# Kernel optimization log

Measured on AMD Instinct MI355X. Metric: run time of the kernel, lower is better.

## Reference

```python
import jax, jax.numpy as jnp
import numpy as np

NUM_NODES = 50000
NUM_EDGES = 800000
INPUT_DIM = 128
HIDDEN_DIM = 128
PE_DIM = 64


def setup_inputs() -> dict:
    key = jax.random.key(0)
    ks = jax.random.split(key, 12)
    x = jax.random.normal(ks[0], (NUM_NODES, INPUT_DIM), dtype=jnp.float32)
    edge_index = jax.random.randint(ks[1], (2, NUM_EDGES), 0, NUM_NODES, dtype=jnp.int64)
    edge_pe = jax.random.normal(ks[2], (NUM_EDGES, PE_DIM), dtype=jnp.float32)
    # message_net: Linear(input+pe -> hidden), ReLU, Linear(hidden -> hidden)
    s1 = 1.0 / np.sqrt(INPUT_DIM + PE_DIM)
    W1 = jax.random.uniform(ks[3], (INPUT_DIM + PE_DIM, HIDDEN_DIM), minval=-s1, maxval=s1)
    b1 = jax.random.uniform(ks[4], (HIDDEN_DIM,), minval=-s1, maxval=s1)
    s2 = 1.0 / np.sqrt(HIDDEN_DIM)
    W2 = jax.random.uniform(ks[5], (HIDDEN_DIM, HIDDEN_DIM), minval=-s2, maxval=s2)
    b2 = jax.random.uniform(ks[6], (HIDDEN_DIM,), minval=-s2, maxval=s2)
    # update_net: Linear(input+hidden -> hidden), ReLU, Linear(hidden -> input)
    s3 = 1.0 / np.sqrt(INPUT_DIM + HIDDEN_DIM)
    U1 = jax.random.uniform(ks[7], (INPUT_DIM + HIDDEN_DIM, HIDDEN_DIM), minval=-s3, maxval=s3)
    c1 = jax.random.uniform(ks[8], (HIDDEN_DIM,), minval=-s3, maxval=s3)
    U2 = jax.random.uniform(ks[9], (HIDDEN_DIM, INPUT_DIM), minval=-s2, maxval=s2)
    c2 = jax.random.uniform(ks[10], (INPUT_DIM,), minval=-s2, maxval=s2)
    return {"x": x, "edge_pe": edge_pe, "W1": W1, "b1": b1, "W2": W2, "b2": b2,
            "U1": U1, "c1": c1, "U2": U2, "c2": c2, "edge_index": edge_index}


def reference(x, edge_pe, W1, b1, W2, b2, U1, c1, U2, c2, edge_index):
    src, dst = edge_index[0], edge_index[1]
    # gather source node features per edge: [E, input_dim]
    msg_in = jnp.concatenate([x[src], edge_pe], axis=-1)  # [E, input+pe]
    h = jax.nn.relu(msg_in @ W1 + b1)
    messages = h @ W2 + b2  # [E, hidden]
    # scatter-add messages to destination nodes
    aggregated = jax.ops.segment_sum(messages, dst, num_segments=x.shape[0])  # [N, hidden]
    upd_in = jnp.concatenate([x, aggregated], axis=-1)  # [N, input+hidden]
    u = jax.nn.relu(upd_in @ U1 + c1)
    return u @ U2 + c2  # [N, input_dim]
```

## Files before the change

kernel.cpp:

```cpp
#include <hip/hip_runtime.h>

#define NN 50000
#define NE 800000

typedef __attribute__((ext_vector_type(8))) short bf16x8;
typedef __attribute__((ext_vector_type(4))) float f32x4;

#define SWS(s, kt) ((s) ^ (((s) >> 3) & 6) ^ ((kt) & 3))

__device__ __forceinline__ unsigned cvtpk(float lo, float hi) {
    unsigned r;
    asm("v_cvt_pk_bf16_f32 %0, %1, %2" : "=v"(r) : "v"(lo), "v"(hi));
    return r;
}
__device__ __forceinline__ uint2 pack4(float a, float b, float c, float d) {
    return make_uint2(cvtpk(a, b), cvtpk(c, d));
}

__device__ __forceinline__ void prep_weights_body(int tid,
        const float* __restrict__ W1, const float* __restrict__ W2,
        const float* __restrict__ U1, const float* __restrict__ U2,
        unsigned short* __restrict__ ws) {
    const float* src; unsigned short* dst; int K;
    if (tid < 6144)        { src = W1; dst = ws;         K = 192; }
    else if (tid < 10240)  { tid -= 6144;  src = W2; dst = ws + 24576; K = 128; }
    else if (tid < 18432)  { tid -= 10240; src = U1; dst = ws + 40960; K = 256; }
    else if (tid < 22528)  { tid -= 18432; src = U2; dst = ws + 73728; K = 128; }
    else return;
    const int m = tid & 127, k = (tid >> 7) * 4;
    const int KT = K >> 5;
    uint2 p = pack4(src[(k + 0) * 128 + m], src[(k + 1) * 128 + m],
                    src[(k + 2) * 128 + m], src[(k + 3) * 128 + m]);
    const int mt = m >> 4, kt = k >> 5, lane = (m & 15) + (((k & 31) >> 3) << 4);
    const int off = (((mt * KT + kt) << 9) + (lane << 3) + ((k & 4) ? 4 : 0));
    *reinterpret_cast<uint2*>(dst + off) = p;
}

__global__ __launch_bounds__(256)
void prep_all(const float* __restrict__ W1, const float* __restrict__ W2,
              const float* __restrict__ U1, const float* __restrict__ U2,
              const float* __restrict__ x, const int* __restrict__ ei,
              unsigned short* __restrict__ ws, unsigned short* __restrict__ xb,
              int* __restrict__ counts) {
    const int b = blockIdx.x;
    if (b < 88) {
        prep_weights_body(b * 256 + threadIdx.x, W1, W2, U1, U2, ws);
    } else if (b < 3213) {
        const int i = ((b - 88) * 256 + threadIdx.x) * 8;
        if (i >= NN * 128) return;
        const float4 a = *reinterpret_cast<const float4*>(&x[i]);
        const float4 c = *reinterpret_cast<const float4*>(&x[i + 4]);
        *reinterpret_cast<uint4*>(&xb[i]) =
            make_uint4(cvtpk(a.x, a.y), cvtpk(a.z, a.w), cvtpk(c.x, c.y), cvtpk(c.z, c.w));
    } else {
        const int e = (b - 3213) * 256 + threadIdx.x;
        if (e < NE) atomicAdd(&counts[ei[NE + e]], 1);
    }
}

__global__ void prep_weights(const float* __restrict__ W1, const float* __restrict__ W2,
                             const float* __restrict__ U1, const float* __restrict__ U2,
                             unsigned short* __restrict__ ws) {
    prep_weights_body(blockIdx.x * blockDim.x + threadIdx.x, W1, W2, U1, U2, ws);
}

__global__ void hist_kernel(const int* __restrict__ ei, int* __restrict__ counts) {
    const int e = blockIdx.x * blockDim.x + threadIdx.x;
    if (e < NE) atomicAdd(&counts[ei[NE + e]], 1);
}

__global__ __launch_bounds__(256)
void scan1_kernel(const int* __restrict__ counts, int* __restrict__ offs,
                  int* __restrict__ bsums) {
    __shared__ int wsum[4];
    const int t = threadIdx.x, lane = t & 63, w = t >> 6;
    const int i = blockIdx.x * 256 + t;
    const int v = (i < NN) ? counts[i] : 0;
    int s = v;
#pragma unroll
    for (int d = 1; d < 64; d <<= 1) {
        int u = __shfl_up(s, d, 64);
        if (lane >= d) s += u;
    }
    if (lane == 63) wsum[w] = s;
    __syncthreads();
    if (t == 0) {
        int a = 0;
#pragma unroll
        for (int k = 0; k < 4; ++k) { int tmp = wsum[k]; wsum[k] = a; a += tmp; }
    }
    __syncthreads();
    const int excl = wsum[w] + s - v;
    if (i < NN) offs[i] = excl;
    if (t == 255) bsums[blockIdx.x] = wsum[3] + s;
}

__global__ __launch_bounds__(256)
void scan2_kernel(const int* __restrict__ bsums, int* __restrict__ boffs) {
    __shared__ int wsum[4];
    const int t = threadIdx.x, lane = t & 63, w = t >> 6;
    const int v = (t < 196) ? bsums[t] : 0;
    int s = v;
#pragma unroll
    for (int d = 1; d < 64; d <<= 1) {
        int u = __shfl_up(s, d, 64);
        if (lane >= d) s += u;
    }
    if (lane == 63) wsum[w] = s;
    __syncthreads();
    if (t == 0) {
        int a = 0;
#pragma unroll
        for (int k = 0; k < 4; ++k) { int tmp = wsum[k]; wsum[k] = a; a += tmp; }
    }
    __syncthreads();
    boffs[t] = wsum[w] + s - v;
}

__global__ __launch_bounds__(256)
void scan3_kernel(int* __restrict__ offs, const int* __restrict__ boffs,
                  int* __restrict__ cursor) {
    const int i = blockIdx.x * 256 + threadIdx.x;
    if (i < NN) {
        const int o = offs[i] + boffs[i >> 8];
        offs[i] = o;
        cursor[i] = o;
    }
}

__global__ void fill_kernel(const int* __restrict__ ei, int* __restrict__ cursor,
                            int* __restrict__ csrpos) {
    const int e = blockIdx.x * blockDim.x + threadIdx.x;
    if (e < NE) csrpos[e] = atomicAdd(&cursor[ei[NE + e]], 1);
}

template <int XBF>
__global__ __launch_bounds__(512)
void edge_kernel2(const float* __restrict__ x,
                  const unsigned short* __restrict__ xb,
                  const float* __restrict__ pe,
                  const float* __restrict__ b1,
                  const float* __restrict__ b2,
                  const int* __restrict__ ei,
                  const int* __restrict__ csrpos,
                  const unsigned short* __restrict__ wf,
                  unsigned short* __restrict__ msg)
{
    __shared__ __align__(16) unsigned char Asw[24576];
    __shared__ __align__(16) unsigned char Hsw[16384];

    const int t = threadIdx.x;
    const int l = t & 63;
    const int w = t >> 6;
    const int g = l >> 4;

    bf16x8 w1r[6], w2r[4];
    {
        const bf16x8* wp1 = reinterpret_cast<const bf16x8*>(wf);
        const bf16x8* wp2 = reinterpret_cast<const bf16x8*>(wf + 24576);
#pragma unroll
        for (int kt = 0; kt < 6; ++kt) w1r[kt] = wp1[(w * 6 + kt) * 64 + l];
#pragma unroll
        for (int kt = 0; kt < 4; ++kt) w2r[kt] = wp2[(w * 4 + kt) * 64 + l];
    }
    const float4 b1v = *reinterpret_cast<const float4*>(&b1[16 * w + 4 * g]);
    const float4 b2v = *reinterpret_cast<const float4*>(&b2[16 * w + 4 * g]);

    const int le = t >> 3;
    const int sub = t & 7;
    const int nt_s = le >> 4;
    const int lane_s = (le & 15) + ((sub & 3) << 4);

    uint4  rxb[2];
    float4 rxf[4];
    float4 rpf[2];

    const int tile0 = blockIdx.x * 5;

    {
        const int e0 = tile0 * 64;
        const int src = ei[e0 + le];
        if constexpr (XBF) {
#pragma unroll
            for (int j = 0; j < 2; ++j)
                rxb[j] = *reinterpret_cast<const uint4*>(&xb[(size_t)src * 128 + sub * 8 + 64 * j]);
        } else {
#pragma unroll
            for (int j = 0; j < 2; ++j) {
                rxf[2 * j]     = *reinterpret_cast<const float4*>(&x[(size_t)src * 128 + sub * 8 + 64 * j]);
                rxf[2 * j + 1] = *reinterpret_cast<const float4*>(&x[(size_t)src * 128 + sub * 8 + 64 * j + 4]);
            }
        }
        rpf[0] = *reinterpret_cast<const float4*>(&pe[(size_t)(e0 + le) * 64 + sub * 8]);
        rpf[1] = *reinterpret_cast<const float4*>(&pe[(size_t)(e0 + le) * 64 + sub * 8 + 4]);
    }

    for (int ti = 0; ti < 5; ++ti) {
        const int e0 = (tile0 + ti) * 64;
        int cp[4];
#pragma unroll
        for (int nt = 0; nt < 4; ++nt) cp[nt] = csrpos[e0 + nt * 16 + (l & 15)];

        __syncthreads();

        {
#pragma unroll
            for (int j = 0; j < 2; ++j) {
                const int kt = (sub >> 2) + 2 * j;
                uint4 v;
                if constexpr (XBF) v = rxb[j];
                else v = make_uint4(cvtpk(rxf[2 * j].x, rxf[2 * j].y), cvtpk(rxf[2 * j].z, rxf[2 * j].w),
                                    cvtpk(rxf[2 * j + 1].x, rxf[2 * j + 1].y), cvtpk(rxf[2 * j + 1].z, rxf[2 * j + 1].w));
                *reinterpret_cast<uint4*>(Asw + ((kt * 4 + nt_s) << 10) + (SWS(lane_s, kt) << 4)) = v;
            }
            const int ktp = 4 + (sub >> 2);
            *reinterpret_cast<uint4*>(Asw + ((ktp * 4 + nt_s) << 10) + (SWS(lane_s, ktp) << 4)) =
                make_uint4(cvtpk(rpf[0].x, rpf[0].y), cvtpk(rpf[0].z, rpf[0].w),
                           cvtpk(rpf[1].x, rpf[1].y), cvtpk(rpf[1].z, rpf[1].w));
        }

        if (ti < 4) {
            const int e0n = e0 + 64;
            const int srcn = ei[e0n + le];
            if constexpr (XBF) {
#pragma unroll
                for (int j = 0; j < 2; ++j)
                    rxb[j] = *reinterpret_cast<const uint4*>(&xb[(size_t)srcn * 128 + sub * 8 + 64 * j]);
            } else {
#pragma unroll
                for (int j = 0; j < 2; ++j) {
                    rxf[2 * j]     = *reinterpret_cast<const float4*>(&x[(size_t)srcn * 128 + sub * 8 + 64 * j]);
                    rxf[2 * j + 1] = *reinterpret_cast<const float4*>(&x[(size_t)srcn * 128 + sub * 8 + 64 * j + 4]);
                }
            }
            rpf[0] = *reinterpret_cast<const float4*>(&pe[(size_t)(e0n + le) * 64 + sub * 8]);
            rpf[1] = *reinterpret_cast<const float4*>(&pe[(size_t)(e0n + le) * 64 + sub * 8 + 4]);
        }

        __syncthreads();

        f32x4 acc[4];
#pragma unroll
        for (int nt = 0; nt < 4; ++nt) acc[nt] = (f32x4){0.f, 0.f, 0.f, 0.f};
#pragma unroll
        for (int kt = 0; kt < 6; ++kt) {
#pragma unroll
            for (int nt = 0; nt < 4; ++nt) {
                const bf16x8 af = *reinterpret_cast<const bf16x8*>(
                    Asw + ((kt * 4 + nt) << 10) + (SWS(l, kt) << 4));
                acc[nt] = __builtin_amdgcn_mfma_f32_16x16x32_bf16(w1r[kt], af, acc[nt], 0, 0, 0);
            }
        }

        {
            const int kt2 = (16 * w + 4 * g) >> 5;
            const int lane2 = (l & 15) + ((2 * (w & 1) + (g >> 1)) << 4);
            const int bo = (g & 1) << 3;
#pragma unroll
            for (int nt = 0; nt < 4; ++nt) {
                float v0 = fmaxf(acc[nt][0] + b1v.x, 0.f);
                float v1 = fmaxf(acc[nt][1] + b1v.y, 0.f);
                float v2 = fmaxf(acc[nt][2] + b1v.z, 0.f);
                float v3 = fmaxf(acc[nt][3] + b1v.w, 0.f);
                *reinterpret_cast<uint2*>(Hsw + ((kt2 * 4 + nt) << 10) + (SWS(lane2, kt2) << 4) + bo) =
                    make_uint2(cvtpk(v0, v1), cvtpk(v2, v3));
            }
        }

        __syncthreads();

#pragma unroll
        for (int nt = 0; nt < 4; ++nt) acc[nt] = (f32x4){0.f, 0.f, 0.f, 0.f};
#pragma unroll
        for (int kt = 0; kt < 4; ++kt) {
#pragma unroll
            for (int nt = 0; nt < 4; ++nt) {
                const bf16x8 hf = *reinterpret_cast<const bf16x8*>(
                    Hsw + ((kt * 4 + nt) << 10) + (SWS(l, kt) << 4));
                acc[nt] = __builtin_amdgcn_mfma_f32_16x16x32_bf16(w2r[kt], hf, acc[nt], 0, 0, 0);
            }
        }

        const int mbase = 16 * w + 4 * g;
#pragma unroll
        for (int nt = 0; nt < 4; ++nt) {
            *reinterpret_cast<uint2*>(&msg[(size_t)cp[nt] * 128 + mbase]) =
                make_uint2(cvtpk(acc[nt][0] + b2v.x, acc[nt][1] + b2v.y),
                           cvtpk(acc[nt][2] + b2v.z, acc[nt][3] + b2v.w));
        }
    }
}

template <int XBF>
__global__ __launch_bounds__(512)
void node_fused(const float* __restrict__ x,
                const unsigned short* __restrict__ xb,
                const float* __restrict__ c1,
                const float* __restrict__ c2,
                const unsigned short* __restrict__ wf,
                const int* __restrict__ offs,
                const int* __restrict__ counts,
                const unsigned short* __restrict__ msg,
                float* __restrict__ out)
{
    __shared__ __align__(16) unsigned char Asw[32768];
    __shared__ __align__(16) unsigned char Hsw[16384];

    const int t = threadIdx.x;
    const int l = t & 63;
    const int w = t >> 6;
    const int g = l >> 4;

    bf16x8 u1r[8], u2r[4];
    {
        const bf16x8* up1 = reinterpret_cast<const bf16x8*>(wf + 40960);
        const bf16x8* up2 = reinterpret_cast<const bf16x8*>(wf + 73728);
#pragma unroll
        for (int kt = 0; kt < 8; ++kt) u1r[kt] = up1[(w * 8 + kt) * 64 + l];
#pragma unroll
        for (int kt = 0; kt < 4; ++kt) u2r[kt] = up2[(w * 4 + kt) * 64 + l];
    }
    const float4 c1v = *reinterpret_cast<const float4*>(&c1[16 * w + 4 * g]);
    const float4 c2v = *reinterpret_cast<const float4*>(&c2[16 * w + 4 * g]);

    const int n0 = blockIdx.x * 64;
    const int le = t >> 3;
    const int q  = t & 7;
    const int nt_s = le >> 4;
    const int node = n0 + le;
    const bool valid = node < NN;

    float a16[16];
#pragma unroll
    for (int i = 0; i < 16; ++i) a16[i] = 0.f;
    int start = 0, cnt = 0;
    if (valid) { start = offs[node]; cnt = counts[node]; }
    for (int j = 0; j < cnt; ++j) {
        const uint4* mp = reinterpret_cast<const uint4*>(&msg[(size_t)(start + j) * 128 + q * 16]);
        const uint4 u0 = mp[0], u1 = mp[1];
        const unsigned arr[8] = {u0.x, u0.y, u0.z, u0.w, u1.x, u1.y, u1.z, u1.w};
#pragma unroll
        for (int r = 0; r < 8; ++r) {
            union { unsigned u; float f; } lo, hi;
            lo.u = arr[r] << 16;
            hi.u = arr[r] & 0xFFFF0000u;
            a16[2 * r]     += lo.f;
            a16[2 * r + 1] += hi.f;
        }
    }

#pragma unroll
    for (int i = 0; i < 2; ++i) {
        const int o = 2 * q + i;
        const int kt = o >> 2;
        const int slot = (le & 15) + ((o & 3) << 4);
        uint4 v = make_uint4(0u, 0u, 0u, 0u);
        if (valid) {
            if constexpr (XBF) {
                v = *reinterpret_cast<const uint4*>(&xb[(size_t)node * 128 + o * 8]);
            } else {
                const float4 f0 = *reinterpret_cast<const float4*>(&x[(size_t)node * 128 + o * 8]);
                const float4 f1 = *reinterpret_cast<const float4*>(&x[(size_t)node * 128 + o * 8 + 4]);
                v = make_uint4(cvtpk(f0.x, f0.y), cvtpk(f0.z, f0.w),
                               cvtpk(f1.x, f1.y), cvtpk(f1.z, f1.w));
            }
        }
        *reinterpret_cast<uint4*>(Asw + ((kt * 4 + nt_s) << 10) + (SWS(slot, kt) << 4)) = v;
    }

    {
        const int kt = 4 + (q >> 1);
#pragma unroll
        for (int i = 0; i < 2; ++i) {
            const int j4 = 2 * (q & 1) + i;
            const int slot = (le & 15) + (j4 << 4);
            *reinterpret_cast<uint4*>(Asw + ((kt * 4 + nt_s) << 10) + (SWS(slot, kt) << 4)) =
                make_uint4(cvtpk(a16[8 * i + 0], a16[8 * i + 1]), cvtpk(a16[8 * i + 2], a16[8 * i + 3]),
                           cvtpk(a16[8 * i + 4], a16[8 * i + 5]), cvtpk(a16[8 * i + 6], a16[8 * i + 7]));
        }
    }
    __syncthreads();

    f32x4 acc[4];
#pragma unroll
    for (int nt = 0; nt < 4; ++nt) acc[nt] = (f32x4){0.f, 0.f, 0.f, 0.f};
#pragma unroll
    for (int kt = 0; kt < 8; ++kt) {
#pragma unroll
        for (int nt = 0; nt < 4; ++nt) {
            const bf16x8 af = *reinterpret_cast<const bf16x8*>(
                Asw + ((kt * 4 + nt) << 10) + (SWS(l, kt) << 4));
            acc[nt] = __builtin_amdgcn_mfma_f32_16x16x32_bf16(u1r[kt], af, acc[nt], 0, 0, 0);
        }
    }

    {
        const int kt2 = (16 * w + 4 * g) >> 5;
        const int lane2 = (l & 15) + ((2 * (w & 1) + (g >> 1)) << 4);
        const int bo = (g & 1) << 3;
#pragma unroll
        for (int nt = 0; nt < 4; ++nt) {
            float v0 = fmaxf(acc[nt][0] + c1v.x, 0.f);
            float v1 = fmaxf(acc[nt][1] + c1v.y, 0.f);
            float v2 = fmaxf(acc[nt][2] + c1v.z, 0.f);
            float v3 = fmaxf(acc[nt][3] + c1v.w, 0.f);
            *reinterpret_cast<uint2*>(Hsw + ((kt2 * 4 + nt) << 10) + (SWS(lane2, kt2) << 4) + bo) =
                make_uint2(cvtpk(v0, v1), cvtpk(v2, v3));
        }
    }
    __syncthreads();

    f32x4 a2[4];
#pragma unroll
    for (int nt = 0; nt < 4; ++nt) a2[nt] = (f32x4){0.f, 0.f, 0.f, 0.f};
#pragma unroll
    for (int kt = 0; kt < 4; ++kt) {
#pragma unroll
        for (int nt = 0; nt < 4; ++nt) {
            const bf16x8 hf = *reinterpret_cast<const bf16x8*>(
                Hsw + ((kt * 4 + nt) << 10) + (SWS(l, kt) << 4));
            a2[nt] = __builtin_amdgcn_mfma_f32_16x16x32_bf16(u2r[kt], hf, a2[nt], 0, 0, 0);
        }
    }

    const int mbase = 16 * w + 4 * g;
#pragma unroll
    for (int nt = 0; nt < 4; ++nt) {
        const int n = n0 + nt * 16 + (l & 15);
        if (n < NN) {
            float4 o;
            o.x = a2[nt][0] + c2v.x;
            o.y = a2[nt][1] + c2v.y;
            o.z = a2[nt][2] + c2v.z;
            o.w = a2[nt][3] + c2v.w;
            *reinterpret_cast<float4*>(&out[(size_t)n * 128 + mbase]) = o;
        }
    }
}

__global__ __launch_bounds__(256)
void edge_atomic(const float* __restrict__ x, const float* __restrict__ pe,
                 const float* __restrict__ b1, const float* __restrict__ b2,
                 const int* __restrict__ ei, const unsigned short* __restrict__ wf,
                 float* __restrict__ agg)
{
    __shared__ __align__(16) unsigned char smem[24576 + 16384];
    unsigned char* Asw = smem;
    unsigned char* Hsw = smem + 24576;

    const int t = threadIdx.x;
    const int l = t & 63;
    const int w = t >> 6;
    const int g = l >> 4;

    bf16x8 w1r[2][6], w2r[2][4];
    {
        const bf16x8* wp1 = reinterpret_cast<const bf16x8*>(wf);
        const bf16x8* wp2 = reinterpret_cast<const bf16x8*>(wf + 24576);
#pragma unroll
        for (int dm = 0; dm < 2; ++dm) {
            const int mt = 2 * w + dm;
#pragma unroll
            for (int kt = 0; kt < 6; ++kt) w1r[dm][kt] = wp1[(mt * 6 + kt) * 64 + l];
#pragma unroll
            for (int kt = 0; kt < 4; ++kt) w2r[dm][kt] = wp2[(mt * 4 + kt) * 64 + l];
        }
    }
    float4 b1v[2], b2v[2];
#pragma unroll
    for (int dm = 0; dm < 2; ++dm) {
        b1v[dm] = *reinterpret_cast<const float4*>(&b1[32 * w + 16 * dm + 4 * g]);
        b2v[dm] = *reinterpret_cast<const float4*>(&b2[32 * w + 16 * dm + 4 * g]);
    }

    const int le = t >> 2;
    const int lq = (t & 3) * 4;
    const int nt_s = le >> 4;

    for (int tile = blockIdx.x * 5; tile < blockIdx.x * 5 + 5; ++tile) {
        const int e0 = tile * 64;
        const int src = ei[e0 + le];
#pragma unroll
        for (int j = 0; j < 12; ++j) {
            const int k = lq + 16 * j;
            float4 av;
            if (j < 8) av = *reinterpret_cast<const float4*>(&x[(size_t)src * 128 + k]);
            else       av = *reinterpret_cast<const float4*>(&pe[(size_t)(e0 + le) * 64 + (k - 128)]);
            const int kt = k >> 5;
            const int lane = (le & 15) + (((k & 31) >> 3) << 4);
            const int off = ((kt * 4 + nt_s) << 10) + (lane << 4) + ((k & 4) << 1);
            *reinterpret_cast<uint2*>(Asw + off) = pack4(av.x, av.y, av.z, av.w);
        }
        int dstv[4];
#pragma unroll
        for (int nt = 0; nt < 4; ++nt) dstv[nt] = ei[NE + e0 + nt * 16 + (l & 15)];
        __syncthreads();

        f32x4 acc[2][4];
#pragma unroll
        for (int dm = 0; dm < 2; ++dm)
#pragma unroll
            for (int nt = 0; nt < 4; ++nt) acc[dm][nt] = (f32x4){0.f, 0.f, 0.f, 0.f};
#pragma unroll
        for (int kt = 0; kt < 6; ++kt) {
#pragma unroll
            for (int nt = 0; nt < 4; ++nt) {
                const bf16x8 af = *reinterpret_cast<const bf16x8*>(Asw + ((kt * 4 + nt) << 10) + (l << 4));
                acc[0][nt] = __builtin_amdgcn_mfma_f32_16x16x32_bf16(w1r[0][kt], af, acc[0][nt], 0, 0, 0);
                acc[1][nt] = __builtin_amdgcn_mfma_f32_16x16x32_bf16(w1r[1][kt], af, acc[1][nt], 0, 0, 0);
            }
        }
#pragma unroll
        for (int dm = 0; dm < 2; ++dm) {
            const float bb[4] = {b1v[dm].x, b1v[dm].y, b1v[dm].z, b1v[dm].w};
            const int lane2 = (l & 15) + ((2 * dm + (g >> 1)) << 4);
#pragma unroll
            for (int nt = 0; nt < 4; ++nt) {
                float v0 = fmaxf(acc[dm][nt][0] + bb[0], 0.f);
                float v1 = fmaxf(acc[dm][nt][1] + bb[1], 0.f);
                float v2 = fmaxf(acc[dm][nt][2] + bb[2], 0.f);
                float v3 = fmaxf(acc[dm][nt][3] + bb[3], 0.f);
                const int off = ((w * 4 + nt) << 10) + (lane2 << 4) + ((g & 1) << 3);
                *reinterpret_cast<uint2*>(Hsw + off) = pack4(v0, v1, v2, v3);
            }
        }
        __syncthreads();

        f32x4 acc2[2][4];
#pragma unroll
        for (int dm = 0; dm < 2; ++dm)
#pragma unroll
            for (int nt = 0; nt < 4; ++nt) acc2[dm][nt] = (f32x4){0.f, 0.f, 0.f, 0.f};
#pragma unroll
        for (int kt = 0; kt < 4; ++kt) {
#pragma unroll
            for (int nt = 0; nt < 4; ++nt) {
                const bf16x8 hf = *reinterpret_cast<const bf16x8*>(Hsw + ((kt * 4 + nt) << 10) + (l << 4));
                acc2[0][nt] = __builtin_amdgcn_mfma_f32_16x16x32_bf16(w2r[0][kt], hf, acc2[0][nt], 0, 0, 0);
                acc2[1][nt] = __builtin_amdgcn_mfma_f32_16x16x32_bf16(w2r[1][kt], hf, acc2[1][nt], 0, 0, 0);
            }
        }
#pragma unroll
        for (int dm = 0; dm < 2; ++dm) {
            const float bb[4] = {b2v[dm].x, b2v[dm].y, b2v[dm].z, b2v[dm].w};
            const int mbase = 32 * w + 16 * dm + 4 * g;
#pragma unroll
            for (int nt = 0; nt < 4; ++nt) {
                float* ap = &agg[(size_t)dstv[nt] * 128 + mbase];
                atomicAdd(ap + 0, acc2[dm][nt][0] + bb[0]);
                atomicAdd(ap + 1, acc2[dm][nt][1] + bb[1]);
                atomicAdd(ap + 2, acc2[dm][nt][2] + bb[2]);
                atomicAdd(ap + 3, acc2[dm][nt][3] + bb[3]);
            }
        }
    }
}

__global__ __launch_bounds__(256)
void node_legacy(const float* __restrict__ x,
                 const float* __restrict__ c1,
                 const float* __restrict__ c2,
                 const unsigned short* __restrict__ wf,
                 float* __restrict__ out)
{
    __shared__ __align__(16) unsigned char smem[32768 + 16384];
    unsigned char* Asw = smem;
    unsigned char* Hsw = smem + 32768;

    const int t = threadIdx.x;
    const int l = t & 63;
    const int w = t >> 6;
    const int g = l >> 4;

    bf16x8 u1r[2][8], u2r[2][4];
    {
        const bf16x8* up1 = reinterpret_cast<const bf16x8*>(wf + 40960);
        const bf16x8* up2 = reinterpret_cast<const bf16x8*>(wf + 73728);
#pragma unroll
        for (int dm = 0; dm < 2; ++dm) {
            const int mt = 2 * w + dm;
#pragma unroll
            for (int kt = 0; kt < 8; ++kt) u1r[dm][kt] = up1[(mt * 8 + kt) * 64 + l];
#pragma unroll
            for (int kt = 0; kt < 4; ++kt) u2r[dm][kt] = up2[(mt * 4 + kt) * 64 + l];
        }
    }
    float4 c1v[2], c2v[2];
#pragma unroll
    for (int dm = 0; dm < 2; ++dm) {
        c1v[dm] = *reinterpret_cast<const float4*>(&c1[32 * w + 16 * dm + 4 * g]);
        c2v[dm] = *reinterpret_cast<const float4*>(&c2[32 * w + 16 * dm + 4 * g]);
    }

    const int n0 = blockIdx.x * 64;
    const int le = t >> 2;
    const int lq = (t & 3) * 4;
    const int nt_s = le >> 4;
    const int node = n0 + le;
    const bool valid = node < NN;

#pragma unroll
    for (int j = 0; j < 16; ++j) {
        const int k = lq + 16 * j;
        float4 av = make_float4(0.f, 0.f, 0.f, 0.f);
        if (valid) {
            if (j < 8) av = *reinterpret_cast<const float4*>(&x[(size_t)node * 128 + k]);
            else       av = *reinterpret_cast<const float4*>(&out[(size_t)node * 128 + (k - 128)]);
        }
        const int kt = k >> 5;
        const int lane = (le & 15) + (((k & 31) >> 3) << 4);
        const int off = ((kt * 4 + nt_s) << 10) + (lane << 4) + ((k & 4) << 1);
        *reinterpret_cast<uint2*>(Asw + off) = pack4(av.x, av.y, av.z, av.w);
    }
    __syncthreads();

    f32x4 acc[2][4];
#pragma unroll
    for (int dm = 0; dm < 2; ++dm)
#pragma unroll
        for (int nt = 0; nt < 4; ++nt) acc[dm][nt] = (f32x4){0.f, 0.f, 0.f, 0.f};
#pragma unroll
    for (int kt = 0; kt < 8; ++kt) {
        bf16x8 af[4];
#pragma unroll
        for (int nt = 0; nt < 4; ++nt)
            af[nt] = *reinterpret_cast<const bf16x8*>(Asw + ((kt * 4 + nt) << 10) + (l << 4));
#pragma unroll
        for (int nt = 0; nt < 4; ++nt) {
            acc[0][nt] = __builtin_amdgcn_mfma_f32_16x16x32_bf16(u1r[0][kt], af[nt], acc[0][nt], 0, 0, 0);
            acc[1][nt] = __builtin_amdgcn_mfma_f32_16x16x32_bf16(u1r[1][kt], af[nt], acc[1][nt], 0, 0, 0);
        }
    }

#pragma unroll
    for (int dm = 0; dm < 2; ++dm) {
        const float bb[4] = {c1v[dm].x, c1v[dm].y, c1v[dm].z, c1v[dm].w};
        const int lane2 = (l & 15) + ((2 * dm + (g >> 1)) << 4);
#pragma unroll
        for (int nt = 0; nt < 4; ++nt) {
            float v0 = fmaxf(acc[dm][nt][0] + bb[0], 0.f);
            float v1 = fmaxf(acc[dm][nt][1] + bb[1], 0.f);
            float v2 = fmaxf(acc[dm][nt][2] + bb[2], 0.f);
            float v3 = fmaxf(acc[dm][nt][3] + bb[3], 0.f);
            const int off = ((w * 4 + nt) << 10) + (lane2 << 4) + ((g & 1) << 3);
            *reinterpret_cast<uint2*>(Hsw + off) = pack4(v0, v1, v2, v3);
        }
    }
    __syncthreads();

    f32x4 acc2[2][4];
#pragma unroll
    for (int dm = 0; dm < 2; ++dm)
#pragma unroll
        for (int nt = 0; nt < 4; ++nt) acc2[dm][nt] = (f32x4){0.f, 0.f, 0.f, 0.f};
#pragma unroll
    for (int kt = 0; kt < 4; ++kt) {
        bf16x8 hf[4];
#pragma unroll
        for (int nt = 0; nt < 4; ++nt)
            hf[nt] = *reinterpret_cast<const bf16x8*>(Hsw + ((kt * 4 + nt) << 10) + (l << 4));
#pragma unroll
        for (int nt = 0; nt < 4; ++nt) {
            acc2[0][nt] = __builtin_amdgcn_mfma_f32_16x16x32_bf16(u2r[0][kt], hf[nt], acc2[0][nt], 0, 0, 0);
            acc2[1][nt] = __builtin_amdgcn_mfma_f32_16x16x32_bf16(u2r[1][kt], hf[nt], acc2[1][nt], 0, 0, 0);
        }
    }

#pragma unroll
    for (int dm = 0; dm < 2; ++dm) {
        const int mbase = 32 * w + 16 * dm + 4 * g;
#pragma unroll
        for (int nt = 0; nt < 4; ++nt) {
            const int n = n0 + nt * 16 + (l & 15);
            if (n < NN) {
                float4 o;
                o.x = acc2[dm][nt][0] + c2v[dm].x;
                o.y = acc2[dm][nt][1] + c2v[dm].y;
                o.z = acc2[dm][nt][2] + c2v[dm].z;
                o.w = acc2[dm][nt][3] + c2v[dm].w;
                *reinterpret_cast<float4*>(&out[(size_t)n * 128 + mbase]) = o;
            }
        }
    }
}

extern "C" void kernel_launch(void* const* d_in, const int* in_sizes, int n_in,
                              void* d_out, int out_size, void* d_ws, size_t ws_size,
                              hipStream_t stream) {
    const float* x  = (const float*)d_in[0];
    const float* pe = (const float*)d_in[1];
    const float* W1 = (const float*)d_in[2];
    const float* b1 = (const float*)d_in[3];
    const float* W2 = (const float*)d_in[4];
    const float* b2 = (const float*)d_in[5];
    const float* U1 = (const float*)d_in[6];
    const float* c1 = (const float*)d_in[7];
    const float* U2 = (const float*)d_in[8];
    const float* c2 = (const float*)d_in[9];
    const int*   ei = (const int*)d_in[10];
    float* out = (float*)d_out;

    const size_t MB = 1 << 20;
    unsigned short* wf = (unsigned short*)d_ws;
    int* counts = (int*)((char*)d_ws + 1 * MB);
    int* offs   = (int*)((char*)d_ws + 1 * MB + 256 * 1024);
    int* cursor = (int*)((char*)d_ws + 1 * MB + 512 * 1024);
    int* bsums  = (int*)((char*)d_ws + 1 * MB + 768 * 1024);
    int* boffs  = (int*)((char*)d_ws + 1 * MB + 772 * 1024);
    int* csrpos = (int*)((char*)d_ws + 2 * MB);
    unsigned short* xb   = (unsigned short*)((char*)d_ws + 6 * MB);
    unsigned short* msgA = (unsigned short*)((char*)d_ws + 19 * MB);
    unsigned short* msgB = (unsigned short*)((char*)d_ws + 6 * MB);

    const size_t MSG_BYTES = (size_t)NE * 128 * 2;
    const size_t REQA = 19 * MB + MSG_BYTES;
    const size_t REQB = 6 * MB + MSG_BYTES;

    if (ws_size >= REQB) {
        const bool tierA = ws_size >= REQA;
        unsigned short* msg = tierA ? msgA : msgB;

        hipMemsetAsync(counts, 0, 50176 * sizeof(int), stream);
        if (tierA) {
            prep_all<<<6338, 256, 0, stream>>>(W1, W2, U1, U2, x, ei, wf, xb, counts);
        } else {
            prep_weights<<<88, 256, 0, stream>>>(W1, W2, U1, U2, wf);
            hist_kernel<<<NE / 256, 256, 0, stream>>>(ei, counts);
        }
        scan1_kernel<<<196, 256, 0, stream>>>(counts, offs, bsums);
        scan2_kernel<<<1, 256, 0, stream>>>(bsums, boffs);
        scan3_kernel<<<196, 256, 0, stream>>>(offs, boffs, cursor);
        fill_kernel<<<NE / 256, 256, 0, stream>>>(ei, cursor, csrpos);
        if (tierA) {
            edge_kernel2<1><<<NE / 64 / 5, 512, 0, stream>>>(x, xb, pe, b1, b2, ei, csrpos, wf, msg);
            node_fused<1><<<(NN + 63) / 64, 512, 0, stream>>>(x, xb, c1, c2, wf, offs, counts, msg, out);
        } else {
            edge_kernel2<0><<<NE / 64 / 5, 512, 0, stream>>>(x, nullptr, pe, b1, b2, ei, csrpos, wf, msg);
            node_fused<0><<<(NN + 63) / 64, 512, 0, stream>>>(x, nullptr, c1, c2, wf, offs, counts, msg, out);
        }
    } else {
        prep_weights<<<88, 256, 0, stream>>>(W1, W2, U1, U2, wf);
        hipMemsetAsync(out, 0, (size_t)NN * 128 * sizeof(float), stream);
        edge_atomic<<<NE / 64 / 5, 256, 0, stream>>>(x, pe, b1, b2, ei, wf, out);
        node_legacy<<<(NN + 63) / 64, 256, 0, stream>>>(x, c1, c2, wf, out);
    }
}
```

Baseline: 276.4 us.

## Use 32x32x16 MFMA for edge first layer with new weight layout

Switches the edge kernel's first GEMM (W1 over 192-dim concat input) from 16x16x32 bf16 MFMA to 32x32x16 MFMA. Each wave now computes a 32x32 output tile with 12 k-steps, which needs a new W1 fragment layout packed by the prep kernel and a matching shared-memory layout for the gathered inputs. The aim is fewer LDS fragment reads and a higher FLOP-per-instruction MFMA. In exchange each wave holds 12 weight fragments in registers instead of 6, which raises register pressure, and the A/H swizzles have to remain bank-conflict free under the new layout.

```diff
diff --git a/kernel.cpp b/kernel.cpp
--- a/kernel.cpp
+++ b/kernel.cpp
@@ -5,6 +5,7 @@
 
 typedef __attribute__((ext_vector_type(8))) short bf16x8;
 typedef __attribute__((ext_vector_type(4))) float f32x4;
+typedef __attribute__((ext_vector_type(16))) float f32x16;
 
 #define SWS(s, kt) ((s) ^ (((s) >> 3) & 6) ^ ((kt) & 3))
 
@@ -21,12 +22,24 @@
         const float* __restrict__ W1, const float* __restrict__ W2,
         const float* __restrict__ U1, const float* __restrict__ U2,
         unsigned short* __restrict__ ws) {
+    if (tid >= 28672) return;
+    if (tid >= 22528) {
+        tid -= 22528;
+        const int m = tid & 127, k = (tid >> 7) * 4;
+        unsigned short* dst = ws + 90112;
+        uint2 p = pack4(W1[(k + 0) * 128 + m], W1[(k + 1) * 128 + m],
+                        W1[(k + 2) * 128 + m], W1[(k + 3) * 128 + m]);
+        const int mt = m >> 5, kt = k >> 4;
+        const int lane = (m & 31) + (((k >> 3) & 1) << 5);
+        const int off = ((mt * 12 + kt) << 9) + (lane << 3) + (k & 4);
+        *reinterpret_cast<uint2*>(dst + off) = p;
+        return;
+    }
     const float* src; unsigned short* dst; int K;
     if (tid < 6144)        { src = W1; dst = ws;         K = 192; }
     else if (tid < 10240)  { tid -= 6144;  src = W2; dst = ws + 24576; K = 128; }
     else if (tid < 18432)  { tid -= 10240; src = U1; dst = ws + 40960; K = 256; }
-    else if (tid < 22528)  { tid -= 18432; src = U2; dst = ws + 73728; K = 128; }
-    else return;
+    else                   { tid -= 18432; src = U2; dst = ws + 73728; K = 128; }
     const int m = tid & 127, k = (tid >> 7) * 4;
     const int KT = K >> 5;
     uint2 p = pack4(src[(k + 0) * 128 + m], src[(k + 1) * 128 + m],
@@ -43,17 +56,17 @@
               unsigned short* __restrict__ ws, unsigned short* __restrict__ xb,
               int* __restrict__ counts) {
     const int b = blockIdx.x;
-    if (b < 88) {
+    if (b < 112) {
         prep_weights_body(b * 256 + threadIdx.x, W1, W2, U1, U2, ws);
-    } else if (b < 3213) {
-        const int i = ((b - 88) * 256 + threadIdx.x) * 8;
+    } else if (b < 3237) {
+        const int i = ((b - 112) * 256 + threadIdx.x) * 8;
         if (i >= NN * 128) return;
         const float4 a = *reinterpret_cast<const float4*>(&x[i]);
         const float4 c = *reinterpret_cast<const float4*>(&x[i + 4]);
         *reinterpret_cast<uint4*>(&xb[i]) =
             make_uint4(cvtpk(a.x, a.y), cvtpk(a.z, a.w), cvtpk(c.x, c.y), cvtpk(c.z, c.w));
     } else {
-        const int e = (b - 3213) * 256 + threadIdx.x;
+        const int e = (b - 3237) * 256 + threadIdx.x;
         if (e < NE) atomicAdd(&counts[ei[NE + e]], 1);
     }
 }
@@ -136,7 +149,7 @@
 
 template <int XBF>
 __global__ __launch_bounds__(512)
-void edge_kernel2(const float* __restrict__ x,
+void edge_kernel5(const float* __restrict__ x,
                   const unsigned short* __restrict__ xb,
                   const float* __restrict__ pe,
                   const float* __restrict__ b1,
@@ -153,23 +166,29 @@
     const int l = t & 63;
     const int w = t >> 6;
     const int g = l >> 4;
-
-    bf16x8 w1r[6], w2r[4];
+    const int mt  = w >> 1;
+    const int ntw = w & 1;
+
+    bf16x8 w1r[12], w2r[4];
     {
-        const bf16x8* wp1 = reinterpret_cast<const bf16x8*>(wf);
+        const bf16x8* wp1 = reinterpret_cast<const bf16x8*>(wf + 90112);
         const bf16x8* wp2 = reinterpret_cast<const bf16x8*>(wf + 24576);
 #pragma unroll
-        for (int kt = 0; kt < 6; ++kt) w1r[kt] = wp1[(w * 6 + kt) * 64 + l];
+        for (int kt = 0; kt < 12; ++kt) w1r[kt] = wp1[(mt * 12 + kt) * 64 + l];
 #pragma unroll
         for (int kt = 0; kt < 4; ++kt) w2r[kt] = wp2[(w * 4 + kt) * 64 + l];
     }
-    const float4 b1v = *reinterpret_cast<const float4*>(&b1[16 * w + 4 * g]);
+    const int mb1 = 32 * mt + 4 * (l >> 5);
+    float4 b1q[4];
+#pragma unroll
+    for (int q = 0; q < 4; ++q)
+        b1q[q] = *reinterpret_cast<const float4*>(&b1[mb1 + 8 * q]);
     const float4 b2v = *reinterpret_cast<const float4*>(&b2[16 * w + 4 * g]);
 
     const int le = t >> 3;
     const int sub = t & 7;
-    const int nt_s = le >> 4;
-    const int lane_s = (le & 15) + ((sub & 3) << 4);
+    const int nt_s32 = le >> 5;
+    const int lane_s32 = (le & 31) + ((sub & 1) << 5);
 
     uint4  rxb[2];
     float4 rxf[4];
@@ -206,15 +225,15 @@
         {
 #pragma unroll
             for (int j = 0; j < 2; ++j) {
-                const int kt = (sub >> 2) + 2 * j;
+                const int kt = (sub >> 1) + 4 * j;
                 uint4 v;
                 if constexpr (XBF) v = rxb[j];
                 else v = make_uint4(cvtpk(rxf[2 * j].x, rxf[2 * j].y), cvtpk(rxf[2 * j].z, rxf[2 * j].w),
                                     cvtpk(rxf[2 * j + 1].x, rxf[2 * j + 1].y), cvtpk(rxf[2 * j + 1].z, rxf[2 * j + 1].w));
-                *reinterpret_cast<uint4*>(Asw + ((kt * 4 + nt_s) << 10) + (SWS(lane_s, kt) << 4)) = v;
-            }
-            const int ktp = 4 + (sub >> 2);
-            *reinterpret_cast<uint4*>(Asw + ((ktp * 4 + nt_s) << 10) + (SWS(lane_s, ktp) << 4)) =
+                *reinterpret_cast<uint4*>(Asw + ((kt * 2 + nt_s32) << 10) + (SWS(lane_s32, kt) << 4)) = v;
+            }
+            const int ktp = 8 + (sub >> 1);
+            *reinterpret_cast<uint4*>(Asw + ((ktp * 2 + nt_s32) << 10) + (SWS(lane_s32, ktp) << 4)) =
                 make_uint4(cvtpk(rpf[0].x, rpf[0].y), cvtpk(rpf[0].z, rpf[0].w),
                            cvtpk(rpf[1].x, rpf[1].y), cvtpk(rpf[1].z, rpf[1].w));
         }
@@ -239,36 +258,35 @@
 
         __syncthreads();
 
+        f32x16 acc1;
+#pragma unroll
+        for (int i = 0; i < 16; ++i) acc1[i] = 0.f;
+#pragma unroll
+        for (int kt = 0; kt < 12; ++kt) {
+            const bf16x8 bf = *reinterpret_cast<const bf16x8*>(
+                Asw + ((kt * 2 + ntw) << 10) + (SWS(l, kt) << 4));
+            acc1 = __builtin_amdgcn_mfma_f32_32x32x16_bf16(w1r[kt], bf, acc1, 0, 0, 0);
+        }
+
+        {
+            const int edge_l = 32 * ntw + (l & 31);
+            const int nt16 = edge_l >> 4;
+            const int bo = (l >> 5) << 3;
+#pragma unroll
+            for (int q = 0; q < 4; ++q) {
+                float v0 = fmaxf(acc1[4 * q + 0] + b1q[q].x, 0.f);
+                float v1 = fmaxf(acc1[4 * q + 1] + b1q[q].y, 0.f);
+                float v2 = fmaxf(acc1[4 * q + 2] + b1q[q].z, 0.f);
+                float v3 = fmaxf(acc1[4 * q + 3] + b1q[q].w, 0.f);
+                const int slot = (l & 15) + (q << 4);
+                *reinterpret_cast<uint2*>(Hsw + ((mt * 4 + nt16) << 10) + (SWS(slot, mt) << 4) + bo) =
+                    make_uint2(cvtpk(v0, v1), cvtpk(v2, v3));
+            }
+        }
+
+        __syncthreads();
+
         f32x4 acc[4];
-#pragma unroll
-        for (int nt = 0; nt < 4; ++nt) acc[nt] = (f32x4){0.f, 0.f, 0.f, 0.f};
-#pragma unroll
-        for (int kt = 0; kt < 6; ++kt) {
-#pragma unroll
-            for (int nt = 0; nt < 4; ++nt) {
-                const bf16x8 af = *reinterpret_cast<const bf16x8*>(
-                    Asw + ((kt * 4 + nt) << 10) + (SWS(l, kt) << 4));
-                acc[nt] = __builtin_amdgcn_mfma_f32_16x16x32_bf16(w1r[kt], af, acc[nt], 0, 0, 0);
-            }
-        }
-
-        {
-            const int kt2 = (16 * w + 4 * g) >> 5;
-            const int lane2 = (l & 15) + ((2 * (w & 1) + (g >> 1)) << 4);
-            const int bo = (g & 1) << 3;
-#pragma unroll
-            for (int nt = 0; nt < 4; ++nt) {
-                float v0 = fmaxf(acc[nt][0] + b1v.x, 0.f);
-                float v1 = fmaxf(acc[nt][1] + b1v.y, 0.f);
-                float v2 = fmaxf(acc[nt][2] + b1v.z, 0.f);
-                float v3 = fmaxf(acc[nt][3] + b1v.w, 0.f);
-                *reinterpret_cast<uint2*>(Hsw + ((kt2 * 4 + nt) << 10) + (SWS(lane2, kt2) << 4) + bo) =
-                    make_uint2(cvtpk(v0, v1), cvtpk(v2, v3));
-            }
-        }
-
-        __syncthreads();
-
 #pragma unroll
         for (int nt = 0; nt < 4; ++nt) acc[nt] = (f32x4){0.f, 0.f, 0.f, 0.f};
 #pragma unroll
@@ -722,9 +740,9 @@
 
         hipMemsetAsync(counts, 0, 50176 * sizeof(int), stream);
         if (tierA) {
-            prep_all<<<6338, 256, 0, stream>>>(W1, W2, U1, U2, x, ei, wf, xb, counts);
+            prep_all<<<6362, 256, 0, stream>>>(W1, W2, U1, U2, x, ei, wf, xb, counts);
         } else {
-            prep_weights<<<88, 256, 0, stream>>>(W1, W2, U1, U2, wf);
+            prep_weights<<<112, 256, 0, stream>>>(W1, W2, U1, U2, wf);
             hist_kernel<<<NE / 256, 256, 0, stream>>>(ei, counts);
         }
         scan1_kernel<<<196, 256, 0, stream>>>(counts, offs, bsums);
@@ -732,14 +750,14 @@
         scan3_kernel<<<196, 256, 0, stream>>>(offs, boffs, cursor);
         fill_kernel<<<NE / 256, 256, 0, stream>>>(ei, cursor, csrpos);
         if (tierA) {
-            edge_kernel2<1><<<NE / 64 / 5, 512, 0, stream>>>(x, xb, pe, b1, b2, ei, csrpos, wf, msg);
+            edge_kernel5<1><<<NE / 64 / 5, 512, 0, stream>>>(x, xb, pe, b1, b2, ei, csrpos, wf, msg);
             node_fused<1><<<(NN + 63) / 64, 512, 0, stream>>>(x, xb, c1, c2, wf, offs, counts, msg, out);
         } else {
-            edge_kernel2<0><<<NE / 64 / 5, 512, 0, stream>>>(x, nullptr, pe, b1, b2, ei, csrpos, wf, msg);
+            edge_kernel5<0><<<NE / 64 / 5, 512, 0, stream>>>(x, nullptr, pe, b1, b2, ei, csrpos, wf, msg);
             node_fused<0><<<(NN + 63) / 64, 512, 0, stream>>>(x, nullptr, c1, c2, wf, offs, counts, msg, out);
         }
     } else {
-        prep_weights<<<88, 256, 0, stream>>>(W1, W2, U1, U2, wf);
+        prep_weights<<<112, 256, 0, stream>>>(W1, W2, U1, U2, wf);
         hipMemsetAsync(out, 0, (size_t)NN * 128 * sizeof(float), stream);
         edge_atomic<<<NE / 64 / 5, 256, 0, stream>>>(x, pe, b1, b2, ei, wf, out);
         node_legacy<<<(NN + 63) / 64, 256, 0, stream>>>(x, c1, c2, wf, out);
```

After: 303.7 us. 1.1x slower.
